# Performance work log

Hardware: AMD Instinct MI355X
Metric: run time of the kernel (lower is better)

Reference implementation:

```python
import jax, jax.numpy as jnp
import numpy as np

N = 50000      # nodes (single node type 'mapping_var')
IN = 128       # in_feats
HID = 128      # hid_feats
OUT = 64       # out_feats
R = 3          # number of relations
E = 800000     # edges per relation (avg degree 16)
NEG_SLOPE = 0.01  # F.leaky_relu default


def setup_inputs() -> dict:
    key = jax.random.key(0)
    ks = jax.random.split(key, 9)
    s = 0.05
    return {
        "x": jax.random.normal(ks[0], (N, IN), jnp.float32),
        "edge_src": jax.random.randint(ks[1], (R, E), 0, N, jnp.int32),
        "edge_dst": jax.random.randint(ks[2], (R, E), 0, N, jnp.int32),
        "W0": jax.random.normal(ks[3], (R, IN, HID), jnp.float32) * s,
        "b0": jnp.zeros((R, HID), jnp.float32),
        "Wl": jax.random.normal(ks[4], (4, R, HID, HID), jnp.float32) * s,
        "bl": jnp.zeros((4, R, HID), jnp.float32),
        "Wout": jax.random.normal(ks[5], (HID, OUT), jnp.float32) * s,
        "bout": jnp.zeros((OUT,), jnp.float32),
    }


def _hetero_conv(h, edge_src, edge_dst, W, b):
    """One HeteroGraphConv layer: per-relation GraphConv (norm='both') then
    mean-aggregate across relations.  h: [N, Din], W: [R, Din, Dout]."""
    ones = jnp.ones((E,), h.dtype)
    outs = []
    for r in range(R):
        src, dst = edge_src[r], edge_dst[r]
        out_deg = jax.ops.segment_sum(ones, src, num_segments=N)
        in_deg = jax.ops.segment_sum(ones, dst, num_segments=N)
        # src-side normalization D_out^{-1/2}
        hn = h * jax.lax.rsqrt(jnp.maximum(out_deg, 1.0))[:, None]
        # gather messages along edges, sum into destinations
        agg = jax.ops.segment_sum(hn[src], dst, num_segments=N)
        # dst-side normalization D_in^{-1/2}
        agg = agg * jax.lax.rsqrt(jnp.maximum(in_deg, 1.0))[:, None]
        outs.append(agg @ W[r] + b[r])
    return jnp.mean(jnp.stack(outs, axis=0), axis=0)  # 'mean' cross-relation aggregate


def reference(x, edge_src, edge_dst, W0, b0, Wl, bl, Wout, bout):
    # Layer 0: in_feats -> hid_feats
    h = _hetero_conv(x, edge_src, edge_dst, W0, b0)
    h = jax.nn.leaky_relu(h, NEG_SLOPE)  # dropout omitted (eval mode)
    # Layers 1..4: hid -> hid; activation after all but the last
    for l in range(4):
        h = _hetero_conv(h, edge_src, edge_dst, Wl[l], bl[l])
        if l != 3:
            h = jax.nn.leaky_relu(h, NEG_SLOPE)
    # final Linear on h['mapping_var']
    return h @ Wout + bout
```

## Files before the change

kernel.cpp:

```cpp
#include <hip/hip_runtime.h>
#include <hip/hip_bf16.h>
#include <cstddef>
#include <cstdint>

#define NNODES 50000
#define NR 3
#define NE 800000
#define HIDF 128
#define OUTF 64
#define NEG_SLOPE 0.01f
#define SCAN_T 1024
#define NCHUNK ((NNODES + SCAN_T - 1) / SCAN_T)
#define KTOT (NR * HIDF)
#define KU (KTOT / 2)
#define RN (NR * NNODES)

__device__ __forceinline__ float bf_lo(uint v) { return __uint_as_float(v << 16); }
__device__ __forceinline__ float bf_hi(uint v) { return __uint_as_float(v & 0xffff0000u); }
__device__ __forceinline__ uint bf_rne(float f) {
    uint u = __float_as_uint(f);
    return (u + 0x7fffu + ((u >> 16) & 1u)) >> 16;
}
__device__ __forceinline__ uint bf_pack(float a, float b) {
    return bf_rne(a) | (bf_rne(b) << 16);
}

typedef short bf16x8 __attribute__((ext_vector_type(8)));
typedef float f32x4 __attribute__((ext_vector_type(4)));
__device__ __forceinline__ bf16x8 as_bf(uint4 v) { return __builtin_bit_cast(bf16x8, v); }

__global__ __launch_bounds__(256) void k_cast_x(const float* __restrict__ x,
                                                uint* __restrict__ xb) {
    int i = blockIdx.x * blockDim.x + threadIdx.x;
    if (i >= NNODES * (HIDF / 2)) return;
    float2 v = *(const float2*)(x + (size_t)i * 2);
    xb[i] = bf_pack(v.x, v.y);
}

__global__ __launch_bounds__(256) void k_cast_w(const float* __restrict__ W0,
                                                const float* __restrict__ Wl,
                                                uint* __restrict__ wbT) {
    int idx = blockIdx.x * blockDim.x + threadIdx.x;
    if (idx >= 5 * HIDF * KU) return;
    int l = idx / (HIDF * KU);
    int rem = idx - l * (HIDF * KU);
    int t = rem / HIDF;
    int n = rem - t * HIDF;
    int r = t / 64;
    int kk = (t - r * 64) * 2;
    const float* Wsrc = (l == 0) ? W0 : Wl + (size_t)(l - 1) * NR * HIDF * HIDF;
    const float* wp = Wsrc + ((size_t)r * HIDF + kk) * HIDF + n;
    float a = wp[0];
    float b = wp[HIDF];
    wbT[(size_t)l * HIDF * KU + (size_t)n * KU + t] = bf_pack(a, b);
}

__global__ __launch_bounds__(256) void k_count(const int* __restrict__ esrc,
                                               const int* __restrict__ edst,
                                               int* __restrict__ deg_out,
                                               int* __restrict__ deg_in,
                                               ushort* __restrict__ epos) {
    int idx = blockIdx.x * blockDim.x + threadIdx.x;
    if (idx >= NR * NE) return;
    int r = idx / NE;
    int s = esrc[idx];
    int d = edst[idx];
    atomicAdd(&deg_out[r * NNODES + s], 1);
    int p = atomicAdd(&deg_in[r * NNODES + d], 1);
    epos[idx] = (ushort)p;
}

__global__ __launch_bounds__(256) void k_norms(const int* __restrict__ deg_out,
                                               const int* __restrict__ deg_in,
                                               float* __restrict__ out_norm,
                                               float* __restrict__ in_norm) {
    int idx = blockIdx.x * blockDim.x + threadIdx.x;
    if (idx >= RN) return;
    int dout = deg_out[idx];
    int din  = deg_in[idx];
    out_norm[idx] = rsqrtf((float)(dout > 1 ? dout : 1));
    in_norm[idx]  = rsqrtf((float)(din  > 1 ? din  : 1));
}

__global__ __launch_bounds__(SCAN_T) void k_scan1(const int* __restrict__ deg_in,
                                                  int* __restrict__ row_ptr,
                                                  int* __restrict__ csums) {
    __shared__ int buf[SCAN_T];
    int r = blockIdx.x / NCHUNK;
    int c = blockIdx.x % NCHUNK;
    int tid = threadIdx.x;
    int i = c * SCAN_T + tid;
    int v = (i < NNODES) ? deg_in[r * NNODES + i] : 0;
    buf[tid] = v;
    __syncthreads();
    for (int off = 1; off < SCAN_T; off <<= 1) {
        int t = (tid >= off) ? buf[tid - off] : 0;
        __syncthreads();
        buf[tid] += t;
        __syncthreads();
    }
    if (i < NNODES) row_ptr[r * (NNODES + 1) + i + 1] = buf[tid];
    if (tid == SCAN_T - 1) csums[r * NCHUNK + c] = buf[SCAN_T - 1];
}

__global__ void k_scan2(const int* __restrict__ csums, int* __restrict__ coffs) {
    int r = threadIdx.x;
    if (r >= NR) return;
    int run = 0;
    for (int c = 0; c < NCHUNK; ++c) {
        coffs[r * NCHUNK + c] = run;
        run += csums[r * NCHUNK + c];
    }
}

__global__ __launch_bounds__(SCAN_T) void k_scan3(int* __restrict__ row_ptr,
                                                  const int* __restrict__ coffs) {
    int r = blockIdx.x / NCHUNK;
    int c = blockIdx.x % NCHUNK;
    int tid = threadIdx.x;
    int i = c * SCAN_T + tid;
    int off = coffs[r * NCHUNK + c];
    if (i < NNODES) row_ptr[r * (NNODES + 1) + i + 1] += off;
    if (tid == 0 && c == 0) row_ptr[r * (NNODES + 1)] = 0;
}

__global__ __launch_bounds__(256) void k_fill_csr(const int* __restrict__ esrc,
                                                  const int* __restrict__ edst,
                                                  const int* __restrict__ row_ptr,
                                                  const ushort* __restrict__ epos,
                                                  const float* __restrict__ out_norm,
                                                  int2* __restrict__ csr_sw) {
    int idx = blockIdx.x * blockDim.x + threadIdx.x;
    if (idx >= NR * NE) return;
    int r = idx / NE;
    int s = esrc[idx];
    int d = edst[idx];
    float w = out_norm[r * NNODES + s];
    int slot = row_ptr[r * (NNODES + 1) + d] + (int)epos[idx];
    csr_sw[(size_t)r * NE + slot] = make_int2(s, __float_as_int(w));
}

__global__ __launch_bounds__(256) void k_aggregate(const uint* __restrict__ hin,
                                                   const float* __restrict__ in_norm,
                                                   const int* __restrict__ row_ptr,
                                                   const int2* __restrict__ csr_sw,
                                                   uint* __restrict__ aggb) {
    int wave = blockIdx.x * 4 + (threadIdx.x >> 6);
    if (wave >= RN) return;
    int r = wave / NNODES;
    int n = wave - r * NNODES;
    int lane = threadIdx.x & 63;
    int quarter = lane >> 4;
    int sub = lane & 15;
    int start = row_ptr[r * (NNODES + 1) + n];
    int end   = row_ptr[r * (NNODES + 1) + n + 1];
    const int2* cw = csr_sw + (size_t)r * NE;

    float acc[8];
#pragma unroll
    for (int k = 0; k < 8; ++k) acc[k] = 0.f;

    int i = start;
    int last = end - 1;
    for (; i + 16 <= end; i += 16) {
        int2 e0 = cw[i + quarter];
        int2 e1 = cw[i + 4 + quarter];
        int2 e2 = cw[i + 8 + quarter];
        int2 e3 = cw[i + 12 + quarter];
        uint4 v0 = *(const uint4*)(hin + (size_t)e0.x * (HIDF / 2) + sub * 4);
        uint4 v1 = *(const uint4*)(hin + (size_t)e1.x * (HIDF / 2) + sub * 4);
        uint4 v2 = *(const uint4*)(hin + (size_t)e2.x * (HIDF / 2) + sub * 4);
        uint4 v3 = *(const uint4*)(hin + (size_t)e3.x * (HIDF / 2) + sub * 4);
        float w0 = __int_as_float(e0.y);
        float w1 = __int_as_float(e1.y);
        float w2 = __int_as_float(e2.y);
        float w3 = __int_as_float(e3.y);
        acc[0] = fmaf(w0, bf_lo(v0.x), acc[0]); acc[1] = fmaf(w0, bf_hi(v0.x), acc[1]);
        acc[2] = fmaf(w0, bf_lo(v0.y), acc[2]); acc[3] = fmaf(w0, bf_hi(v0.y), acc[3]);
        acc[4] = fmaf(w0, bf_lo(v0.z), acc[4]); acc[5] = fmaf(w0, bf_hi(v0.z), acc[5]);
        acc[6] = fmaf(w0, bf_lo(v0.w), acc[6]); acc[7] = fmaf(w0, bf_hi(v0.w), acc[7]);
        acc[0] = fmaf(w1, bf_lo(v1.x), acc[0]); acc[1] = fmaf(w1, bf_hi(v1.x), acc[1]);
        acc[2] = fmaf(w1, bf_lo(v1.y), acc[2]); acc[3] = fmaf(w1, bf_hi(v1.y), acc[3]);
        acc[4] = fmaf(w1, bf_lo(v1.z), acc[4]); acc[5] = fmaf(w1, bf_hi(v1.z), acc[5]);
        acc[6] = fmaf(w1, bf_lo(v1.w), acc[6]); acc[7] = fmaf(w1, bf_hi(v1.w), acc[7]);
        acc[0] = fmaf(w2, bf_lo(v2.x), acc[0]); acc[1] = fmaf(w2, bf_hi(v2.x), acc[1]);
        acc[2] = fmaf(w2, bf_lo(v2.y), acc[2]); acc[3] = fmaf(w2, bf_hi(v2.y), acc[3]);
        acc[4] = fmaf(w2, bf_lo(v2.z), acc[4]); acc[5] = fmaf(w2, bf_hi(v2.z), acc[5]);
        acc[6] = fmaf(w2, bf_lo(v2.w), acc[6]); acc[7] = fmaf(w2, bf_hi(v2.w), acc[7]);
        acc[0] = fmaf(w3, bf_lo(v3.x), acc[0]); acc[1] = fmaf(w3, bf_hi(v3.x), acc[1]);
        acc[2] = fmaf(w3, bf_lo(v3.y), acc[2]); acc[3] = fmaf(w3, bf_hi(v3.y), acc[3]);
        acc[4] = fmaf(w3, bf_lo(v3.z), acc[4]); acc[5] = fmaf(w3, bf_hi(v3.z), acc[5]);
        acc[6] = fmaf(w3, bf_lo(v3.w), acc[6]); acc[7] = fmaf(w3, bf_hi(v3.w), acc[7]);
    }
    for (; i + 8 <= end; i += 8) {
        int2 eA = cw[i + quarter];
        int2 eB = cw[i + 4 + quarter];
        uint4 vA = *(const uint4*)(hin + (size_t)eA.x * (HIDF / 2) + sub * 4);
        uint4 vB = *(const uint4*)(hin + (size_t)eB.x * (HIDF / 2) + sub * 4);
        float wA = __int_as_float(eA.y);
        float wB = __int_as_float(eB.y);
        acc[0] = fmaf(wA, bf_lo(vA.x), acc[0]); acc[1] = fmaf(wA, bf_hi(vA.x), acc[1]);
        acc[2] = fmaf(wA, bf_lo(vA.y), acc[2]); acc[3] = fmaf(wA, bf_hi(vA.y), acc[3]);
        acc[4] = fmaf(wA, bf_lo(vA.z), acc[4]); acc[5] = fmaf(wA, bf_hi(vA.z), acc[5]);
        acc[6] = fmaf(wA, bf_lo(vA.w), acc[6]); acc[7] = fmaf(wA, bf_hi(vA.w), acc[7]);
        acc[0] = fmaf(wB, bf_lo(vB.x), acc[0]); acc[1] = fmaf(wB, bf_hi(vB.x), acc[1]);
        acc[2] = fmaf(wB, bf_lo(vB.y), acc[2]); acc[3] = fmaf(wB, bf_hi(vB.y), acc[3]);
        acc[4] = fmaf(wB, bf_lo(vB.z), acc[4]); acc[5] = fmaf(wB, bf_hi(vB.z), acc[5]);
        acc[6] = fmaf(wB, bf_lo(vB.w), acc[6]); acc[7] = fmaf(wB, bf_hi(vB.w), acc[7]);
    }
    for (; i < end; i += 4) {
        int e_idx = i + quarter;
        bool live = e_idx < end;
        int2 e = cw[live ? e_idx : last];
        float w = live ? __int_as_float(e.y) : 0.f;
        uint4 v = *(const uint4*)(hin + (size_t)e.x * (HIDF / 2) + sub * 4);
        acc[0] = fmaf(w, bf_lo(v.x), acc[0]); acc[1] = fmaf(w, bf_hi(v.x), acc[1]);
        acc[2] = fmaf(w, bf_lo(v.y), acc[2]); acc[3] = fmaf(w, bf_hi(v.y), acc[3]);
        acc[4] = fmaf(w, bf_lo(v.z), acc[4]); acc[5] = fmaf(w, bf_hi(v.z), acc[5]);
        acc[6] = fmaf(w, bf_lo(v.w), acc[6]); acc[7] = fmaf(w, bf_hi(v.w), acc[7]);
    }

#pragma unroll
    for (int k = 0; k < 8; ++k) {
        acc[k] += __shfl_xor(acc[k], 16);
        acc[k] += __shfl_xor(acc[k], 32);
    }

    if (quarter == 0) {
        float wn = in_norm[r * NNODES + n];
        uint4 pk;
        pk.x = bf_pack(acc[0] * wn, acc[1] * wn);
        pk.y = bf_pack(acc[2] * wn, acc[3] * wn);
        pk.z = bf_pack(acc[4] * wn, acc[5] * wn);
        pk.w = bf_pack(acc[6] * wn, acc[7] * wn);
        *(uint4*)(aggb + (size_t)n * KU + r * (HIDF / 2) + sub * 4) = pk;
    }
}

__global__ __launch_bounds__(256) void k_conv_mm(const uint* __restrict__ aggb,
                                                 const uint* __restrict__ wbT,
                                                 const float* __restrict__ bias,
                                                 ushort* __restrict__ hout,
                                                 int act) {
    int wv   = threadIdx.x >> 6;
    int lane = threadIdx.x & 63;
    int lrow = lane & 15;
    int kgrp = lane >> 4;
    int rb = blockIdx.x * 128 + wv * 32;

    f32x4 acc[2][8];
#pragma unroll
    for (int m = 0; m < 2; ++m)
#pragma unroll
        for (int nr = 0; nr < 8; ++nr) acc[m][nr] = (f32x4){0.f, 0.f, 0.f, 0.f};

    int row0 = rb + lrow;
    int row1 = rb + 16 + lrow;
    bool v0 = row0 < NNODES;
    bool v1 = row1 < NNODES;
    const uint* a0p = aggb + (size_t)row0 * KU + kgrp * 4;
    const uint* a1p = aggb + (size_t)row1 * KU + kgrp * 4;
    const uint* bp  = wbT + (size_t)lrow * KU + kgrp * 4;
    const uint4 za = make_uint4(0u, 0u, 0u, 0u);

#pragma unroll
    for (int ks = 0; ks < KTOT / 32; ++ks) {
        uint4 ua0 = v0 ? *(const uint4*)(a0p + ks * 16) : za;
        uint4 ua1 = v1 ? *(const uint4*)(a1p + ks * 16) : za;
        bf16x8 af0 = as_bf(ua0);
        bf16x8 af1 = as_bf(ua1);
#pragma unroll
        for (int nr = 0; nr < 8; ++nr) {
            uint4 ub = *(const uint4*)(bp + (size_t)nr * (16 * KU) + ks * 16);
            bf16x8 bf = as_bf(ub);
            acc[0][nr] = __builtin_amdgcn_mfma_f32_16x16x32_bf16(af0, bf, acc[0][nr], 0, 0, 0);
            acc[1][nr] = __builtin_amdgcn_mfma_f32_16x16x32_bf16(af1, bf, acc[1][nr], 0, 0, 0);
        }
    }

    const float inv3 = 1.f / 3.f;
#pragma unroll
    for (int nr = 0; nr < 8; ++nr) {
        int col = nr * 16 + lrow;
        float bm = (bias[col] + bias[HIDF + col] + bias[2 * HIDF + col]) * inv3;
#pragma unroll
        for (int m = 0; m < 2; ++m) {
            int rbase = rb + m * 16 + kgrp * 4;
#pragma unroll
            for (int i = 0; i < 4; ++i) {
                int row = rbase + i;
                if (row >= NNODES) continue;
                float t = acc[m][nr][i] * inv3 + bm;
                if (act) t = (t > 0.f) ? t : NEG_SLOPE * t;
                hout[(size_t)row * HIDF + col] = (ushort)bf_rne(t);
            }
        }
    }
}

__global__ __launch_bounds__(256) void k_final(const uint* __restrict__ h,
                                               const float* __restrict__ Wout,
                                               const float* __restrict__ bout,
                                               float* __restrict__ out) {
    int tid = threadIdx.x;
    int col = tid & 63;
    int row = blockIdx.x * 4 + (tid >> 6);
    if (row >= NNODES) return;
    const uint* hp = h + (size_t)row * (HIDF / 2);
    float acc = bout[col];
#pragma unroll 8
    for (int ku = 0; ku < HIDF / 2; ++ku) {
        uint v = hp[ku];
        acc = fmaf(bf_lo(v), Wout[(2 * ku) * OUTF + col], acc);
        acc = fmaf(bf_hi(v), Wout[(2 * ku + 1) * OUTF + col], acc);
    }
    out[(size_t)row * OUTF + col] = acc;
}

extern "C" void kernel_launch(void* const* d_in, const int* in_sizes, int n_in,
                              void* d_out, int out_size, void* d_ws, size_t ws_size,
                              hipStream_t stream) {
    const float* x    = (const float*)d_in[0];
    const int*   esrc = (const int*)d_in[1];
    const int*   edst = (const int*)d_in[2];
    const float* W0   = (const float*)d_in[3];
    const float* b0   = (const float*)d_in[4];
    const float* Wl   = (const float*)d_in[5];
    const float* bl   = (const float*)d_in[6];
    const float* Wout = (const float*)d_in[7];
    const float* bout = (const float*)d_in[8];
    float* out = (float*)d_out;

    char* ws = (char*)d_ws;
    size_t off = 0;
    auto carve = [&](size_t bytes) {
        size_t p = off;
        off += (bytes + 255) & ~(size_t)255;
        return p;
    };
    const size_t SZ_RN_I = (size_t)RN * 4;
    size_t o_deg_out = carve(SZ_RN_I);
    size_t o_deg_in  = carve(SZ_RN_I);
    size_t zero_span = off;
    size_t o_out_nrm = carve(SZ_RN_I);
    size_t o_in_nrm  = carve(SZ_RN_I);
    size_t o_row_ptr = carve((size_t)NR * (NNODES + 1) * 4);
    size_t o_csums   = carve((size_t)NR * NCHUNK * 4);
    size_t o_coffs   = carve((size_t)NR * NCHUNK * 4);
    size_t o_csr     = carve((size_t)NR * NE * 8);
    size_t o_epos    = carve((size_t)NR * NE * 2);
    size_t o_aggb    = carve((size_t)NNODES * KU * 4);
    size_t o_xb      = carve((size_t)NNODES * (HIDF / 2) * 4);
    size_t o_h       = carve((size_t)NNODES * (HIDF / 2) * 4);
    size_t o_wbT     = carve((size_t)5 * HIDF * KU * 4);
    (void)ws_size;

    int*    deg_out  = (int*)(ws + o_deg_out);
    int*    deg_in   = (int*)(ws + o_deg_in);
    float*  out_norm = (float*)(ws + o_out_nrm);
    float*  in_norm  = (float*)(ws + o_in_nrm);
    int*    row_ptr  = (int*)(ws + o_row_ptr);
    int*    csums    = (int*)(ws + o_csums);
    int*    coffs    = (int*)(ws + o_coffs);
    int2*   csr_sw   = (int2*)(ws + o_csr);
    ushort* epos     = (ushort*)(ws + o_epos);
    uint*   aggb     = (uint*)(ws + o_aggb);
    uint*   xb       = (uint*)(ws + o_xb);
    uint*   h        = (uint*)(ws + o_h);
    uint*   wbT      = (uint*)(ws + o_wbT);

    hipMemsetAsync(ws, 0, zero_span, stream);

    int nEdgeBlocks = (NR * NE + 255) / 256;
    k_cast_x<<<(NNODES * (HIDF / 2) + 255) / 256, 256, 0, stream>>>(x, xb);
    k_cast_w<<<(5 * HIDF * KU + 255) / 256, 256, 0, stream>>>(W0, Wl, wbT);
    k_count<<<nEdgeBlocks, 256, 0, stream>>>(esrc, edst, deg_out, deg_in, epos);
    k_norms<<<(RN + 255) / 256, 256, 0, stream>>>(deg_out, deg_in, out_norm, in_norm);
    k_scan1<<<NR * NCHUNK, SCAN_T, 0, stream>>>(deg_in, row_ptr, csums);
    k_scan2<<<1, 64, 0, stream>>>(csums, coffs);
    k_scan3<<<NR * NCHUNK, SCAN_T, 0, stream>>>(row_ptr, coffs);
    k_fill_csr<<<nEdgeBlocks, 256, 0, stream>>>(esrc, edst, row_ptr, epos, out_norm, csr_sw);

    const int aggBlocks = (RN + 3) / 4;
    const int mmBlocks  = (NNODES + 127) / 128;

    const uint* hin = xb;
    for (int l = 0; l < 5; ++l) {
        k_aggregate<<<aggBlocks, 256, 0, stream>>>(hin, in_norm, row_ptr, csr_sw, aggb);
        const uint*  Wp = wbT + (size_t)l * HIDF * KU;
        const float* bp = (l == 0) ? b0 : bl + (size_t)(l - 1) * NR * HIDF;
        k_conv_mm<<<mmBlocks, 256, 0, stream>>>(aggb, Wp, bp, (ushort*)h, (l < 4) ? 1 : 0);
        hin = h;
    }
    k_final<<<(NNODES + 3) / 4, 256, 0, stream>>>(h, Wout, bout, out);
}
```

Measured before the change: 1.065 ms.

## Build degree counts and CSR via node-range chunks with shared-memory atomics

Replaces the global-atomic degree count and edge-position CSR fill with kernels where each 1024-thread block owns a 4096-node range. Each block scans every edge of its relation and does the counting and slot assignment with LDS atomics. This removes the memset, the epos buffer and contended global atomics. The cost is that every block re-reads the whole edge array: 13 chunks per relation, roughly 13x redundant edge reads, with only 78 and 39 blocks launched.

```diff
diff --git a/kernel.cpp b/kernel.cpp
--- a/kernel.cpp
+++ b/kernel.cpp
@@ -14,6 +14,8 @@
 #define KTOT (NR * HIDF)
 #define KU (KTOT / 2)
 #define RN (NR * NNODES)
+#define CHN 4096
+#define NCH ((NNODES + CHN - 1) / CHN)
 
 __device__ __forceinline__ float bf_lo(uint v) { return __uint_as_float(v << 16); }
 __device__ __forceinline__ float bf_hi(uint v) { return __uint_as_float(v & 0xffff0000u); }
@@ -55,19 +57,39 @@
     wbT[(size_t)l * HIDF * KU + (size_t)n * KU + t] = bf_pack(a, b);
 }
 
-__global__ __launch_bounds__(256) void k_count(const int* __restrict__ esrc,
-                                               const int* __restrict__ edst,
-                                               int* __restrict__ deg_out,
-                                               int* __restrict__ deg_in,
-                                               ushort* __restrict__ epos) {
-    int idx = blockIdx.x * blockDim.x + threadIdx.x;
-    if (idx >= NR * NE) return;
-    int r = idx / NE;
-    int s = esrc[idx];
-    int d = edst[idx];
-    atomicAdd(&deg_out[r * NNODES + s], 1);
-    int p = atomicAdd(&deg_in[r * NNODES + d], 1);
-    epos[idx] = (ushort)p;
+__global__ __launch_bounds__(1024) void k_chunk_count(const int* __restrict__ esrc,
+                                                      const int* __restrict__ edst,
+                                                      int* __restrict__ deg_out,
+                                                      int* __restrict__ deg_in) {
+    __shared__ int cnt[CHN];
+    int bid = blockIdx.x;
+    int role = bid / (NR * NCH);
+    int rem = bid - role * (NR * NCH);
+    int r = rem / NCH;
+    int c = rem - r * NCH;
+    int lo = c * CHN;
+    int hi = lo + CHN; if (hi > NNODES) hi = NNODES;
+    int span = hi - lo;
+    const int* arr = (role ? esrc : edst) + (size_t)r * NE;
+
+    for (int i = threadIdx.x; i < CHN; i += 1024) cnt[i] = 0;
+    __syncthreads();
+
+    int base = threadIdx.x * 4;
+    for (int it = 0; it < NE; it += 4096) {
+        int idx = it + base;
+        if (idx < NE) {
+            int4 v = *(const int4*)(arr + idx);
+            if ((unsigned)(v.x - lo) < (unsigned)span) atomicAdd(&cnt[v.x - lo], 1);
+            if ((unsigned)(v.y - lo) < (unsigned)span) atomicAdd(&cnt[v.y - lo], 1);
+            if ((unsigned)(v.z - lo) < (unsigned)span) atomicAdd(&cnt[v.z - lo], 1);
+            if ((unsigned)(v.w - lo) < (unsigned)span) atomicAdd(&cnt[v.w - lo], 1);
+        }
+    }
+    __syncthreads();
+
+    int* dst = (role ? deg_out : deg_in) + r * NNODES;
+    for (int i = threadIdx.x; i < span; i += 1024) dst[lo + i] = cnt[i];
 }
 
 __global__ __launch_bounds__(256) void k_norms(const int* __restrict__ deg_out,
@@ -124,20 +146,51 @@
     if (tid == 0 && c == 0) row_ptr[r * (NNODES + 1)] = 0;
 }
 
-__global__ __launch_bounds__(256) void k_fill_csr(const int* __restrict__ esrc,
-                                                  const int* __restrict__ edst,
-                                                  const int* __restrict__ row_ptr,
-                                                  const ushort* __restrict__ epos,
-                                                  const float* __restrict__ out_norm,
-                                                  int2* __restrict__ csr_sw) {
-    int idx = blockIdx.x * blockDim.x + threadIdx.x;
-    if (idx >= NR * NE) return;
-    int r = idx / NE;
-    int s = esrc[idx];
-    int d = edst[idx];
-    float w = out_norm[r * NNODES + s];
-    int slot = row_ptr[r * (NNODES + 1) + d] + (int)epos[idx];
-    csr_sw[(size_t)r * NE + slot] = make_int2(s, __float_as_int(w));
+__global__ __launch_bounds__(1024) void k_chunk_fill(const int* __restrict__ esrc,
+                                                     const int* __restrict__ edst,
+                                                     const int* __restrict__ row_ptr,
+                                                     const float* __restrict__ out_norm,
+                                                     int2* __restrict__ csr_sw) {
+    __shared__ int cur[CHN];
+    int bid = blockIdx.x;
+    int r = bid / NCH;
+    int c = bid - r * NCH;
+    int lo = c * CHN;
+    int hi = lo + CHN; if (hi > NNODES) hi = NNODES;
+    int span = hi - lo;
+    const int* sarr = esrc + (size_t)r * NE;
+    const int* darr = edst + (size_t)r * NE;
+    const int* rp = row_ptr + r * (NNODES + 1);
+    const float* on = out_norm + r * NNODES;
+    int2* cs = csr_sw + (size_t)r * NE;
+
+    for (int i = threadIdx.x; i < CHN; i += 1024) cur[i] = 0;
+    __syncthreads();
+
+    int base = threadIdx.x * 4;
+    for (int it = 0; it < NE; it += 4096) {
+        int idx = it + base;
+        if (idx < NE) {
+            int4 d = *(const int4*)(darr + idx);
+            int4 s = *(const int4*)(sarr + idx);
+            if ((unsigned)(d.x - lo) < (unsigned)span) {
+                int p = atomicAdd(&cur[d.x - lo], 1);
+                cs[rp[d.x] + p] = make_int2(s.x, __float_as_int(on[s.x]));
+            }
+            if ((unsigned)(d.y - lo) < (unsigned)span) {
+                int p = atomicAdd(&cur[d.y - lo], 1);
+                cs[rp[d.y] + p] = make_int2(s.y, __float_as_int(on[s.y]));
+            }
+            if ((unsigned)(d.z - lo) < (unsigned)span) {
+                int p = atomicAdd(&cur[d.z - lo], 1);
+                cs[rp[d.z] + p] = make_int2(s.z, __float_as_int(on[s.z]));
+            }
+            if ((unsigned)(d.w - lo) < (unsigned)span) {
+                int p = atomicAdd(&cur[d.w - lo], 1);
+                cs[rp[d.w] + p] = make_int2(s.w, __float_as_int(on[s.w]));
+            }
+        }
+    }
 }
 
 __global__ __launch_bounds__(256) void k_aggregate(const uint* __restrict__ hin,
@@ -341,14 +394,12 @@
     const size_t SZ_RN_I = (size_t)RN * 4;
     size_t o_deg_out = carve(SZ_RN_I);
     size_t o_deg_in  = carve(SZ_RN_I);
-    size_t zero_span = off;
     size_t o_out_nrm = carve(SZ_RN_I);
     size_t o_in_nrm  = carve(SZ_RN_I);
     size_t o_row_ptr = carve((size_t)NR * (NNODES + 1) * 4);
     size_t o_csums   = carve((size_t)NR * NCHUNK * 4);
     size_t o_coffs   = carve((size_t)NR * NCHUNK * 4);
     size_t o_csr     = carve((size_t)NR * NE * 8);
-    size_t o_epos    = carve((size_t)NR * NE * 2);
     size_t o_aggb    = carve((size_t)NNODES * KU * 4);
     size_t o_xb      = carve((size_t)NNODES * (HIDF / 2) * 4);
     size_t o_h       = carve((size_t)NNODES * (HIDF / 2) * 4);
@@ -363,23 +414,20 @@
     int*    csums    = (int*)(ws + o_csums);
     int*    coffs    = (int*)(ws + o_coffs);
     int2*   csr_sw   = (int2*)(ws + o_csr);
-    ushort* epos     = (ushort*)(ws + o_epos);
     uint*   aggb     = (uint*)(ws + o_aggb);
     uint*   xb       = (uint*)(ws + o_xb);
     uint*   h        = (uint*)(ws + o_h);
     uint*   wbT      = (uint*)(ws + o_wbT);
 
-    hipMemsetAsync(ws, 0, zero_span, stream);
-
-    int nEdgeBlocks = (NR * NE + 255) / 256;
+
     k_cast_x<<<(NNODES * (HIDF / 2) + 255) / 256, 256, 0, stream>>>(x, xb);
     k_cast_w<<<(5 * HIDF * KU + 255) / 256, 256, 0, stream>>>(W0, Wl, wbT);
-    k_count<<<nEdgeBlocks, 256, 0, stream>>>(esrc, edst, deg_out, deg_in, epos);
+    k_chunk_count<<<2 * NR * NCH, 1024, 0, stream>>>(esrc, edst, deg_out, deg_in);
     k_norms<<<(RN + 255) / 256, 256, 0, stream>>>(deg_out, deg_in, out_norm, in_norm);
     k_scan1<<<NR * NCHUNK, SCAN_T, 0, stream>>>(deg_in, row_ptr, csums);
     k_scan2<<<1, 64, 0, stream>>>(csums, coffs);
     k_scan3<<<NR * NCHUNK, SCAN_T, 0, stream>>>(row_ptr, coffs);
-    k_fill_csr<<<nEdgeBlocks, 256, 0, stream>>>(esrc, edst, row_ptr, epos, out_norm, csr_sw);
+    k_chunk_fill<<<NR * NCH, 1024, 0, stream>>>(esrc, edst, row_ptr, out_norm, csr_sw);
 
     const int aggBlocks = (RN + 3) / 4;
     const int mmBlocks  = (NNODES + 127) / 128;
```

Result: slower. 1.308 ms (+22.8%).
